# Optimization experiments

Measured on AMD Instinct MI355X. Metric: run time of the kernel, lower is better.

The kernel has to match this reference:

```python
import jax, jax.numpy as jnp
import numpy as np
from jax import lax

NUM_HEAD = 16; M = 2; N = 2; RP = 16; HNR = 8; WNR = 8; NUM_RATIO = 64
ED = 4096           # origin_embed_dim == resize_embed_dim
HD = 4              # head dim (= ED / (NUM_HEAD * 64))
R = 1024 // RP      # 64
THETA = 10.0


def conv2d(x, w, b, stride, pad):
    y = lax.conv_general_dilated(x, w, (stride, stride), ((pad, pad), (pad, pad)),
                                 dimension_numbers=('NCHW', 'OIHW', 'NCHW'))
    return y + b[None, :, None, None]


def layernorm(x, g, b):
    mu = jnp.mean(x, -1, keepdims=True)
    var = jnp.mean((x - mu) ** 2, -1, keepdims=True)
    return (x - mu) * lax.rsqrt(var + 1e-5) * g + b


def l2norm(x):
    n = jnp.sqrt(jnp.sum(x * x, -1, keepdims=True))
    return x / jnp.maximum(n, 1e-12)


def window_partition(x, m, n):
    B, C, H, W = x.shape
    Hp = ((H + m - 1) // m) * m
    Wp = ((W + n - 1) // n) * n
    x = jnp.pad(x, ((0, 0), (0, 0), (0, Hp - H), (0, Wp - W)))
    wh, ww = Hp // m, Wp // n
    x = x.reshape(B, C, m, wh, n, ww).transpose(0, 2, 4, 1, 3, 5).reshape(B * m * n, C, wh, ww)
    return x, (wh, ww), (Hp, Wp)


def window_reverse(x, m, n, paged_shape):
    Hp, Wp = paged_shape
    Bmn, C, wh, ww = x.shape
    B = Bmn // (m * n)
    return x.reshape(B, m, n, C, wh, ww).transpose(0, 3, 1, 4, 2, 5).reshape(B, C, Hp, Wp)


def rope_rotate(t, h, w, theta):
    # 2D axial RoPE over a (h, w) grid flattened row-major; head dim split
    # half for the h-axis and half for the w-axis, consecutive-pair rotation.
    d = t.shape[-1]; dh = d // 2
    freqs = 1.0 / (theta ** (jnp.arange(0, dh, 2, dtype=jnp.float32) / dh))
    px = jnp.repeat(jnp.arange(h, dtype=jnp.float32), w)
    py = jnp.tile(jnp.arange(w, dtype=jnp.float32), h)
    ang = jnp.concatenate([px[:, None] * freqs, py[:, None] * freqs], -1)  # (h*w, dh)
    cos, sin = jnp.cos(ang), jnp.sin(ang)
    tp = t.reshape(t.shape[:-1] + (dh, 2))
    tr = jnp.stack([tp[..., 0] * cos - tp[..., 1] * sin,
                    tp[..., 0] * sin + tp[..., 1] * cos], -1)
    return tr.reshape(t.shape)


def setup_inputs() -> dict:
    key = jax.random.key(0)
    ks = jax.random.split(key, 12)
    s = 0.05
    inp = {
        'x': jax.random.normal(ks[0], (1, 3, 8, 8), jnp.float32),
        'x_conv_w': jax.random.normal(ks[1], (64, 3, 3, 3), jnp.float32) * s,
        'x_conv_b': jnp.zeros((64,), jnp.float32),
        'r_conv_w': jax.random.normal(ks[2], (64, 3, 3, 3), jnp.float32) * s,
        'r_conv_b': jnp.zeros((64,), jnp.float32),
        'patch_w': jax.random.normal(ks[3], (ED, 64, RP, RP), jnp.float32) * s,
        'patch_b': jnp.zeros((ED,), jnp.float32),
        'b_proj_w': jax.random.normal(ks[4], (HD, HD), jnp.float32) * 0.5,
        'b_proj_b': jnp.zeros((HD,), jnp.float32),
        'q_proj_w': jax.random.normal(ks[5], (HD, HD), jnp.float32) * 0.5,
        'q_proj_b': jnp.zeros((HD,), jnp.float32),
        'norm_b_g': jnp.ones((HD,), jnp.float32),
        'norm_b_b': jnp.zeros((HD,), jnp.float32),
        'norm_q_g': jnp.ones((HD,), jnp.float32),
        'norm_q_b': jnp.zeros((HD,), jnp.float32),
        'q_attn_w': jax.random.normal(ks[6], (1, HD), jnp.float32) * 0.5,
        'q_attn_b': jnp.zeros((1,), jnp.float32),
        'pos': jax.random.normal(ks[7], (1, NUM_HEAD, 65536, HD), jnp.float32),
        'proj_w': jax.random.normal(ks[8], (ED, ED, 1, 1), jnp.float32) * s,
        'proj_b': jnp.zeros((ED,), jnp.float32),
    }
    return inp


def reference(x, x_conv_w, x_conv_b, r_conv_w, r_conv_b, patch_w, patch_b,
              b_proj_w, b_proj_b, q_proj_w, q_proj_b,
              norm_b_g, norm_b_b, norm_q_g, norm_q_b,
              q_attn_w, q_attn_b, pos, proj_w, proj_b):
    B, C, H, W = x.shape
    x_feat = conv2d(x, x_conv_w, x_conv_b, 1, 1)                     # (B,64,H,W)
    x_win, xws, x_shape = window_partition(x_feat, M, N)
    pad_h, pad_w = x_shape[0] - H, x_shape[1] - W
    xp = jnp.pad(x, ((0, 0), (0, 0), (0, pad_h), (0, pad_w)))
    res_x = jax.image.resize(xp, (B, 3, 1024, 1024), method='bilinear')
    res_x = conv2d(res_x, r_conv_w, r_conv_b, 1, 1)                  # (B,64,1024,1024)
    res_x_base = conv2d(res_x, patch_w, patch_b, RP, 0)              # (B,4096,64,64)
    C_idx = ED // NUM_RATIO                                          # 64
    rxr = res_x_base.reshape(B, C_idx, HNR, WNR, R, R)
    rxr = rxr.transpose(0, 1, 4, 2, 5, 3).reshape(B, C_idx, R * HNR, R * WNR)  # (B,64,512,512)
    rx_win, rws, rx_shape = window_partition(rxr, M, N)              # (B*4,64,256,256)
    xw = x_win.reshape(B * M * N, NUM_HEAD, -1, xws[0] * xws[1]).swapaxes(-2, -1)  # (B*4,16,Nb,4)
    rw = rx_win.reshape(B * M * N, NUM_HEAD, -1, rws[0] * rws[1]).swapaxes(-2, -1) # (B*4,16,Nq,4)
    b = layernorm(xw, norm_b_g, norm_b_b) @ b_proj_w.T + b_proj_b
    q = layernorm(rw, norm_q_g, norm_q_b) @ q_proj_w.T + q_proj_b
    b_norm = l2norm(b)
    gate = jax.nn.sigmoid(q @ q_attn_w.T + q_attn_b)                 # (B*4,16,Nq,1)
    q = l2norm(q * gate + pos * (1.0 - gate))
    q_rot = rope_rotate(q, rws[0], rws[1], THETA)
    b_rot = rope_rotate(b_norm, xws[0], xws[1], THETA)
    attn = jnp.einsum('bhqd,bhkd->bhqk', q_rot, b_rot)               # (B*4,16,Nq,Nb)
    out_win = attn @ b                                               # (B*4,16,Nq,4)
    out_win = out_win.swapaxes(-2, -1).reshape(B * M * N, -1, rws[0], rws[1])
    n_x = window_reverse(out_win, M, N, rx_shape)                    # (B,64,512,512)
    n_x = n_x.reshape(B, C_idx, R, HNR, R, WNR).transpose(0, 1, 3, 5, 2, 4).reshape(B, -1, R, R)
    x_final = conv2d(n_x + res_x_base, proj_w, proj_b, 1, 0)         # (B,4096,64,64)
    return (x_final, attn)
```

## Files before the change

kernel.cpp:

```cpp
#include <hip/hip_runtime.h>
#include <hip/hip_bf16.h>
#include <math.h>
#include <cstddef>

#define CB_F     2097152ull
#define BIASC_F  4194304ull
#define BBUF_F   4198400ull
#define BROT_F   4202496ull
#define P_F      4206592ull
#define PB_F     20983808ull
#define PRWB_F   29372416ull
#define ATTN_OFF 16777216ull

typedef __attribute__((ext_vector_type(8))) short bf16x8;
typedef __attribute__((ext_vector_type(4))) float f32x4;

#define GLOAD16(gsrc, ldst) \
  __builtin_amdgcn_global_load_lds((const __attribute__((address_space(1))) void*)(gsrc), \
                                   (__attribute__((address_space(3))) void*)(ldst), 16, 0, 0)

__global__ __launch_bounds__(256) void k_xmap_bchain(
    const float* __restrict__ x, __hip_bfloat16* __restrict__ Xmb,
    const float* __restrict__ xcw, const float* __restrict__ xcb,
    const float* __restrict__ bpw, const float* __restrict__ bpb,
    const float* __restrict__ nbg, const float* __restrict__ nbb,
    float* __restrict__ b_buf, float* __restrict__ b_rot)
{
    __shared__ float xs[3][8][8];
    int t = threadIdx.x;
    if (t < 192) xs[t / 64][(t / 8) % 8][t % 8] = x[t];
    __syncthreads();

    if (blockIdx.x < 4096) {
        int s = blockIdx.x, py = s >> 6, px = s & 63;
        __hip_bfloat16 out4[4];
        #pragma unroll
        for (int u = 0; u < 4; ++u) {
            int k = t * 4 + u;
            float val = 0.0f;
            if (k < 972) {
                int ci = k / 324, r = k % 324, m = r / 18, n = r % 18;
                int row = 16 * py + m - 1, col = 16 * px + n - 1;
                if (row >= 0 && row < 1024 && col >= 0 && col < 1024) {
                    float fu = (row + 0.5f) * 0.0078125f - 0.5f;
                    float fv = (col + 0.5f) * 0.0078125f - 0.5f;
                    float fi = floorf(fu), fj = floorf(fv);
                    float tu = fu - fi, tv = fv - fj;
                    int i0 = (int)fi, j0 = (int)fj;
                    int i0c = min(max(i0, 0), 7), i1c = min(max(i0 + 1, 0), 7);
                    int j0c = min(max(j0, 0), 7), j1c = min(max(j0 + 1, 0), 7);
                    val = (xs[ci][i0c][j0c] * (1.f - tv) + xs[ci][i0c][j1c] * tv) * (1.f - tu)
                        + (xs[ci][i1c][j0c] * (1.f - tv) + xs[ci][i1c][j1c] * tv) * tu;
                }
            }
            out4[u] = __float2bfloat16(val);
        }
        *(ushort4*)(Xmb + (size_t)s * 1024 + t * 4) = *(const ushort4*)out4;
        return;
    }

    __shared__ float xf[64][8][8];
    for (int o = t; o < 4096; o += 256) {
        int c = o >> 6, i = (o >> 3) & 7, j = o & 7;
        float acc = xcb[c];
        for (int ic = 0; ic < 3; ++ic)
            for (int ky = 0; ky < 3; ++ky)
                for (int kx = 0; kx < 3; ++kx) {
                    int ii = i - 1 + ky, jj = j - 1 + kx;
                    if (ii >= 0 && ii < 8 && jj >= 0 && jj < 8)
                        acc = fmaf(xs[ic][ii][jj], xcw[((c * 3 + ic) * 3 + ky) * 3 + kx], acc);
                }
        xf[c][i][j] = acc;
    }
    __syncthreads();
    for (int idx = t; idx < 1024; idx += 256) {
        int wi = idx >> 8, h = (idx >> 4) & 15, pp = idx & 15;
        int pr = pp >> 2, pc = pp & 3;
        int gi = 4 * (wi >> 1) + pr, gj = 4 * (wi & 1) + pc;
        float v[4];
        #pragma unroll
        for (int d = 0; d < 4; ++d) v[d] = xf[h * 4 + d][gi][gj];
        float mu = 0.25f * (v[0] + v[1] + v[2] + v[3]);
        float var = 0.25f * ((v[0]-mu)*(v[0]-mu) + (v[1]-mu)*(v[1]-mu) +
                             (v[2]-mu)*(v[2]-mu) + (v[3]-mu)*(v[3]-mu));
        float inv = rsqrtf(var + 1e-5f);
        float xh[4];
        #pragma unroll
        for (int d = 0; d < 4; ++d) xh[d] = (v[d] - mu) * inv * nbg[d] + nbb[d];
        float bv[4];
        #pragma unroll
        for (int d = 0; d < 4; ++d) {
            float a = bpb[d];
            #pragma unroll
            for (int e = 0; e < 4; ++e) a = fmaf(xh[e], bpw[d * 4 + e], a);
            bv[d] = a;
        }
        #pragma unroll
        for (int d = 0; d < 4; ++d) b_buf[idx * 4 + d] = bv[d];
        float nn = sqrtf(bv[0]*bv[0] + bv[1]*bv[1] + bv[2]*bv[2] + bv[3]*bv[3]);
        float in2 = 1.0f / fmaxf(nn, 1e-12f);
        float bn[4];
        #pragma unroll
        for (int d = 0; d < 4; ++d) bn[d] = bv[d] * in2;
        float s0, c0, s1, c1;
        sincosf((float)pr, &s0, &c0);
        sincosf((float)pc, &s1, &c1);
        b_rot[idx * 4 + 0] = bn[0] * c0 - bn[1] * s0;
        b_rot[idx * 4 + 1] = bn[0] * s0 + bn[1] * c0;
        b_rot[idx * 4 + 2] = bn[2] * c1 - bn[3] * s1;
        b_rot[idx * 4 + 3] = bn[2] * s1 + bn[3] * c1;
    }
}

__global__ __launch_bounds__(256) void k_cmat(
    const float* __restrict__ pw, const float* __restrict__ rcw,
    const float* __restrict__ pb, const float* __restrict__ rcb,
    __hip_bfloat16* __restrict__ Cb, float* __restrict__ biasc)
{
    __shared__ __attribute__((aligned(16))) float Ws[64 * 28];
    __shared__ __attribute__((aligned(16))) float Dz[20 * 20 * 28];
    int t = threadIdx.x;
    int w = t >> 6, lane = t & 63;
    int co = blockIdx.x * 4 + w;
    const float* pwc = pw + (size_t)co * 16384;

    for (int i = t; i < 1728; i += 256) Ws[(i / 27) * 28 + (i % 27)] = rcw[i];
    if (t < 64) Ws[t * 28 + 27] = rcb[t];
    for (int i = t; i < 11200; i += 256) Dz[i] = 0.0f;
    __syncthreads();

    float D[4][27];
    #pragma unroll
    for (int q = 0; q < 4; ++q)
        #pragma unroll
        for (int j = 0; j < 27; ++j) D[q][j] = 0.0f;
    float bsum = 0.0f;
    const float* src = pwc + 4 * lane;
    #pragma unroll 4
    for (int c = 0; c < 64; ++c) {
        f32x4 v = *(const f32x4*)(src + c * 256);
        const f32x4* wp = (const f32x4*)&Ws[c * 28];
        #pragma unroll
        for (int q7 = 0; q7 < 7; ++q7) {
            f32x4 wv = wp[q7];
            #pragma unroll
            for (int e = 0; e < 4; ++e) {
                int j = q7 * 4 + e;
                if (j < 27) {
                    #pragma unroll
                    for (int q = 0; q < 4; ++q)
                        D[q][j] = fmaf(wv[e], v[q], D[q][j]);
                } else {
                    bsum = fmaf(wv[e], v[0] + v[1] + v[2] + v[3], bsum);
                }
            }
        }
    }
    #pragma unroll
    for (int s = 32; s; s >>= 1) bsum += __shfl_down(bsum, s, 64);
    if (lane == 0) biasc[co] = pb[co] + bsum;

    for (int p = 0; p < 4; ++p) {
        __syncthreads();
        if (w == p) {
            #pragma unroll
            for (int q = 0; q < 4; ++q) {
                int rs = 4 * lane + q, r = rs >> 4, s2 = rs & 15;
                float* dst = &Dz[((r + 2) * 20 + (s2 + 2)) * 28];
                #pragma unroll
                for (int j = 0; j < 27; ++j) dst[j] = D[q][j];
            }
        }
        __syncthreads();
        int cop = blockIdx.x * 4 + p;
        if (t < 162) {
            int m = t / 9, n0 = (t % 9) * 2;
            float a0[3] = {}, a1[3] = {};
            #pragma unroll
            for (int ci = 0; ci < 3; ++ci)
                #pragma unroll
                for (int ky = 0; ky < 3; ++ky)
                    #pragma unroll
                    for (int kx = 0; kx < 3; ++kx) {
                        int j = ci * 9 + ky * 3 + kx;
                        const float* pz = &Dz[((m - ky + 2) * 20 + (n0 - kx + 2)) * 28 + j];
                        a0[ci] += pz[0];
                        a1[ci] += pz[28];
                    }
            size_t cb = (size_t)cop * 1024;
            #pragma unroll
            for (int ci = 0; ci < 3; ++ci) {
                Cb[cb + ci * 324 + m * 18 + n0]     = __float2bfloat16(a0[ci]);
                Cb[cb + ci * 324 + m * 18 + n0 + 1] = __float2bfloat16(a1[ci]);
            }
        }
        if (t >= 162 && t < 214)
            Cb[(size_t)cop * 1024 + 972 + (t - 162)] = __float2bfloat16(0.0f);
    }
}

__global__ __launch_bounds__(256) void k_cast_bf16(
    const float* __restrict__ in, __hip_bfloat16* __restrict__ out, long n)
{
    long i = ((long)blockIdx.x * 256 + threadIdx.x) * 8;
    if (i >= n) return;
    float4 v0 = *(const float4*)(in + i);
    float4 v1 = *(const float4*)(in + i + 4);
    __hip_bfloat16 h[8] = {__float2bfloat16(v0.x), __float2bfloat16(v0.y),
                           __float2bfloat16(v0.z), __float2bfloat16(v0.w),
                           __float2bfloat16(v1.x), __float2bfloat16(v1.y),
                           __float2bfloat16(v1.z), __float2bfloat16(v1.w)};
    *(ushort4*)(out + i)     = *(const ushort4*)h;
    *(ushort4*)(out + i + 4) = *(const ushort4*)(h + 4);
}

template <int BIASROW>
__global__ __launch_bounds__(512) void gemm_8p(
    const __hip_bfloat16* __restrict__ A, const __hip_bfloat16* __restrict__ B,
    const float* __restrict__ bias, float* __restrict__ C,
    int M, int N, int K)
{
    __shared__ short lds[65536];
    const short* Ag = (const short*)A;
    const short* Bg = (const short*)B;
    int t = threadIdx.x;
    int lane = t & 63;
    int wid = t >> 6;
    int wm = wid >> 2, wn = wid & 3;

    int nwg = gridDim.x * gridDim.y;
    int flat = blockIdx.y * gridDim.x + blockIdx.x;
    int swz = (flat & 7) * (nwg >> 3) + (flat >> 3);
    int bx = swz % gridDim.x, by = swz / gridDim.x;
    int m0 = by * 256, n0 = bx * 256;
    int T = K >> 6;

    int srow = t >> 3;
    int sc = ((t & 7) ^ (srow & 7)) * 8;
    const short* Asrc[4]; const short* Bsrc[4];
    #pragma unroll
    for (int p = 0; p < 4; ++p) {
        Asrc[p] = Ag + (size_t)(m0 + p * 64 + srow) * K + sc;
        Bsrc[p] = Bg + (size_t)(n0 + p * 64 + srow) * K + sc;
    }

    f32x4 acc[8][4] = {};

    #pragma unroll
    for (int u = 0; u < 2; ++u) {
        short* bA = lds + u * 32768;
        short* bB = bA + 16384;
        size_t ko = (size_t)u * 64;
        #pragma unroll
        for (int p = 0; p < 4; ++p) GLOAD16(Asrc[p] + ko, bA + p * 4096 + t * 8);
        #pragma unroll
        for (int p = 0; p < 4; ++p) GLOAD16(Bsrc[p] + ko, bB + p * 4096 + t * 8);
    }

    for (int tt = 0; tt < T; ++tt) {
        if (tt + 1 < T) { asm volatile("s_waitcnt vmcnt(8)" ::: "memory"); }
        else            { asm volatile("s_waitcnt vmcnt(0)" ::: "memory"); }
        __builtin_amdgcn_s_barrier();
        __builtin_amdgcn_sched_barrier(0);

        const char* Asb = (const char*)(lds + (tt & 1) * 32768);
        const char* Bsb = Asb + 32768;
        short* pA = lds + (tt & 1) * 32768;
        short* pB = pA + 16384;
        bool pf = (tt + 2) < T;
        size_t ko = (size_t)(tt + 2) * 64;

        bf16x8 af[4][2], bfr[4][2];
        #pragma unroll
        for (int f = 0; f < 4; ++f) {
            int r = wm * 128 + f * 16 + (lane & 15);
            #pragma unroll
            for (int ks = 0; ks < 2; ++ks) {
                int cb = ks * 64 + (lane >> 4) * 16;
                af[f][ks] = *(const bf16x8*)(Asb + r * 128 + (cb ^ ((r & 7) << 4)));
            }
        }
        #pragma unroll
        for (int g = 0; g < 2; ++g) {
            int r = wn * 64 + g * 16 + (lane & 15);
            #pragma unroll
            for (int ks = 0; ks < 2; ++ks) {
                int cb = ks * 64 + (lane >> 4) * 16;
                bfr[g][ks] = *(const bf16x8*)(Bsb + r * 128 + (cb ^ ((r & 7) << 4)));
            }
        }
        __builtin_amdgcn_s_barrier();
        __builtin_amdgcn_s_setprio(1);
        #pragma unroll
        for (int f = 0; f < 4; ++f)
            #pragma unroll
            for (int g = 0; g < 2; ++g)
                #pragma unroll
                for (int ks = 0; ks < 2; ++ks)
                    acc[f][g] = __builtin_amdgcn_mfma_f32_16x16x32_bf16(
                        af[f][ks], bfr[g][ks], acc[f][g], 0, 0, 0);
        __builtin_amdgcn_s_setprio(0);
        __builtin_amdgcn_s_barrier();
        #pragma unroll
        for (int g = 2; g < 4; ++g) {
            int r = wn * 64 + g * 16 + (lane & 15);
            #pragma unroll
            for (int ks = 0; ks < 2; ++ks) {
                int cb = ks * 64 + (lane >> 4) * 16;
                bfr[g][ks] = *(const bf16x8*)(Bsb + r * 128 + (cb ^ ((r & 7) << 4)));
            }
        }
        __builtin_amdgcn_s_barrier();
        __builtin_amdgcn_s_setprio(1);
        #pragma unroll
        for (int f = 0; f < 4; ++f)
            #pragma unroll
            for (int g = 2; g < 4; ++g)
                #pragma unroll
                for (int ks = 0; ks < 2; ++ks)
                    acc[f][g] = __builtin_amdgcn_mfma_f32_16x16x32_bf16(
                        af[f][ks], bfr[g][ks], acc[f][g], 0, 0, 0);
        __builtin_amdgcn_s_setprio(0);
        __builtin_amdgcn_s_barrier();
        #pragma unroll
        for (int f = 0; f < 4; ++f) {
            int r = wm * 128 + 64 + f * 16 + (lane & 15);
            #pragma unroll
            for (int ks = 0; ks < 2; ++ks) {
                int cb = ks * 64 + (lane >> 4) * 16;
                af[f][ks] = *(const bf16x8*)(Asb + r * 128 + (cb ^ ((r & 7) << 4)));
            }
        }
        if (pf) {
            #pragma unroll
            for (int p = 0; p < 4; ++p) GLOAD16(Bsrc[p] + ko, pB + p * 4096 + t * 8);
        }
        __builtin_amdgcn_s_barrier();
        __builtin_amdgcn_s_setprio(1);
        #pragma unroll
        for (int f = 0; f < 4; ++f)
            #pragma unroll
            for (int g = 0; g < 2; ++g)
                #pragma unroll
                for (int ks = 0; ks < 2; ++ks)
                    acc[4 + f][g] = __builtin_amdgcn_mfma_f32_16x16x32_bf16(
                        af[f][ks], bfr[g][ks], acc[4 + f][g], 0, 0, 0);
        __builtin_amdgcn_s_setprio(0);
        __builtin_amdgcn_s_barrier();
        if (pf) {
            #pragma unroll
            for (int p = 0; p < 4; ++p) GLOAD16(Asrc[p] + ko, pA + p * 4096 + t * 8);
        }
        __builtin_amdgcn_s_setprio(1);
        #pragma unroll
        for (int f = 0; f < 4; ++f)
            #pragma unroll
            for (int g = 2; g < 4; ++g)
                #pragma unroll
                for (int ks = 0; ks < 2; ++ks)
                    acc[4 + f][g] = __builtin_amdgcn_mfma_f32_16x16x32_bf16(
                        af[f][ks], bfr[g][ks], acc[4 + f][g], 0, 0, 0);
        __builtin_amdgcn_s_setprio(0);
    }

    #pragma unroll
    for (int f = 0; f < 8; ++f) {
        #pragma unroll
        for (int g = 0; g < 4; ++g) {
            int col = n0 + wn * 64 + g * 16 + (lane & 15);
            #pragma unroll
            for (int rg = 0; rg < 4; ++rg) {
                int row = m0 + wm * 128 + f * 16 + (lane >> 4) * 4 + rg;
                float bb = BIASROW ? bias[row] : bias[col];
                C[(size_t)row * N + col] = acc[f][g][rg] + bb;
            }
        }
    }
}

__global__ __launch_bounds__(256) void k_attn(
    const float* __restrict__ P, const float* __restrict__ b_buf, const float* __restrict__ b_rot,
    const float* __restrict__ qpw, const float* __restrict__ qpb,
    const float* __restrict__ nqg, const float* __restrict__ nqb,
    const float* __restrict__ qaw, const float* __restrict__ qab,
    const float* __restrict__ pos, __hip_bfloat16* __restrict__ Pb,
    float* __restrict__ attn_out)
{
    __shared__ float bs[16][4], brs[16][4];
    int t = threadIdx.x;
    int wh = blockIdx.y;
    int wi = wh >> 4, h = wh & 15;
    if (t < 64) {
        ((float*)bs)[t]  = b_buf[wh * 64 + t];
        ((float*)brs)[t] = b_rot[wh * 64 + t];
    }
    __syncthreads();
    int p = blockIdx.x * 256 + t;
    int wr = p >> 8, wc = p & 255;
    int gr = ((wi >> 1) << 8) + wr, gc = ((wi & 1) << 8) + wc;
    int y = gr >> 3, hnr = gr & 7, xq = gc >> 3, wnr = gc & 7;
    size_t base = (size_t)(y * 64 + xq) * 4096 + h * 256 + hnr * 8 + wnr;
    float r[4];
    #pragma unroll
    for (int d = 0; d < 4; ++d) r[d] = P[base + (size_t)d * 64];
    float mu = 0.25f * (r[0] + r[1] + r[2] + r[3]);
    float var = 0.25f * ((r[0]-mu)*(r[0]-mu) + (r[1]-mu)*(r[1]-mu) +
                         (r[2]-mu)*(r[2]-mu) + (r[3]-mu)*(r[3]-mu));
    float inv = rsqrtf(var + 1e-5f);
    float xh[4];
    #pragma unroll
    for (int d = 0; d < 4; ++d) xh[d] = (r[d] - mu) * inv * nqg[d] + nqb[d];
    float q4[4];
    #pragma unroll
    for (int d = 0; d < 4; ++d) {
        float a = qpb[d];
        #pragma unroll
        for (int e = 0; e < 4; ++e) a = fmaf(xh[e], qpw[d * 4 + e], a);
        q4[d] = a;
    }
    float z = qab[0];
    #pragma unroll
    for (int d = 0; d < 4; ++d) z = fmaf(q4[d], qaw[d], z);
    float gate = 1.0f / (1.0f + expf(-z));
    float4 pv = *(const float4*)(pos + ((size_t)h * 65536 + p) * 4);
    float v[4];
    v[0] = q4[0] * gate + pv.x * (1.0f - gate);
    v[1] = q4[1] * gate + pv.y * (1.0f - gate);
    v[2] = q4[2] * gate + pv.z * (1.0f - gate);
    v[3] = q4[3] * gate + pv.w * (1.0f - gate);
    float nn = sqrtf(v[0]*v[0] + v[1]*v[1] + v[2]*v[2] + v[3]*v[3]);
    float in2 = 1.0f / fmaxf(nn, 1e-12f);
    #pragma unroll
    for (int d = 0; d < 4; ++d) v[d] *= in2;
    float s0, c0, s1, c1;
    sincosf((float)wr, &s0, &c0);
    sincosf((float)wc, &s1, &c1);
    float qr[4];
    qr[0] = v[0] * c0 - v[1] * s0;
    qr[1] = v[0] * s0 + v[1] * c0;
    qr[2] = v[2] * c1 - v[3] * s1;
    qr[3] = v[2] * s1 + v[3] * c1;
    float arow[16];
    #pragma unroll
    for (int k = 0; k < 16; ++k)
        arow[k] = qr[0] * brs[k][0] + qr[1] * brs[k][1] + qr[2] * brs[k][2] + qr[3] * brs[k][3];
    size_t abase = ((size_t)wh * 65536 + p) * 16;
    #pragma unroll
    for (int kq = 0; kq < 4; ++kq) {
        float4 av;
        av.x = arow[kq * 4 + 0]; av.y = arow[kq * 4 + 1];
        av.z = arow[kq * 4 + 2]; av.w = arow[kq * 4 + 3];
        *(float4*)(attn_out + abase + kq * 4) = av;
    }
    float o[4] = {0.f, 0.f, 0.f, 0.f};
    #pragma unroll
    for (int k = 0; k < 16; ++k) {
        #pragma unroll
        for (int d = 0; d < 4; ++d) o[d] = fmaf(arow[k], bs[k][d], o[d]);
    }
    #pragma unroll
    for (int d = 0; d < 4; ++d)
        Pb[base + (size_t)d * 64] = __float2bfloat16(r[d] + o[d]);
}

extern "C" void kernel_launch(void* const* d_in, const int* in_sizes, int n_in,
                              void* d_out, int out_size, void* d_ws, size_t ws_size,
                              hipStream_t stream)
{
    (void)in_sizes; (void)n_in; (void)out_size; (void)ws_size;
    const float* x    = (const float*)d_in[0];
    const float* xcw  = (const float*)d_in[1];
    const float* xcb  = (const float*)d_in[2];
    const float* rcw  = (const float*)d_in[3];
    const float* rcb  = (const float*)d_in[4];
    const float* pw   = (const float*)d_in[5];
    const float* pb   = (const float*)d_in[6];
    const float* bpw  = (const float*)d_in[7];
    const float* bpb  = (const float*)d_in[8];
    const float* qpw  = (const float*)d_in[9];
    const float* qpb  = (const float*)d_in[10];
    const float* nbg  = (const float*)d_in[11];
    const float* nbb  = (const float*)d_in[12];
    const float* nqg  = (const float*)d_in[13];
    const float* nqb  = (const float*)d_in[14];
    const float* qaw  = (const float*)d_in[15];
    const float* qab  = (const float*)d_in[16];
    const float* pos  = (const float*)d_in[17];
    const float* prw  = (const float*)d_in[18];
    const float* prb  = (const float*)d_in[19];

    float* ws = (float*)d_ws;
    __hip_bfloat16* Xmb   = (__hip_bfloat16*)d_ws;
    __hip_bfloat16* Cb    = (__hip_bfloat16*)(ws + CB_F);
    float*          biasc = ws + BIASC_F;
    float*          b_buf = ws + BBUF_F;
    float*          b_rot = ws + BROT_F;
    float*          P     = ws + P_F;
    __hip_bfloat16* Pb    = (__hip_bfloat16*)(ws + PB_F);
    __hip_bfloat16* prwb  = (__hip_bfloat16*)(ws + PRWB_F);
    float* out = (float*)d_out;

    k_xmap_bchain<<<4097, 256, 0, stream>>>(x, Xmb, xcw, xcb, bpw, bpb, nbg, nbb,
                                            b_buf, b_rot);
    k_cmat<<<1024, 256, 0, stream>>>(pw, rcw, pb, rcb, Cb, biasc);
    gemm_8p<0><<<dim3(16, 16), 512, 0, stream>>>(Xmb, Cb, biasc, P, 4096, 4096, 1024);
    k_attn<<<dim3(256, 64), 256, 0, stream>>>(P, b_buf, b_rot, qpw, qpb, nqg, nqb,
                                              qaw, qab, pos, Pb, out + ATTN_OFF);
    k_cast_bf16<<<8192, 256, 0, stream>>>(prw, prwb, 16777216L);
    gemm_8p<1><<<dim3(16, 16), 512, 0, stream>>>(prwb, Pb, prb, out, 4096, 4096, 4096);
}
```

Baseline: 492.7 us.

## Split k_cmat work across two waves per output channel and shrink LDS staging

Each block of k_cmat now handles 2 output channels instead of 4, with two waves splitting each channel's 256 spatial positions, which halves the per-thread D accumulator from 4x27 to 2x27 floats. The LDS staging buffer shrinks from 28 to 12 floats per position by scattering one input channel at a time across 6 passes, and the bias partial sums are combined through a small shared array. The grid doubles to 2048 blocks. The aim is lower register and LDS pressure so more waves fit per CU, at the cost of more barrier-separated passes and redundant Ws and Dz initialisation per block.

```diff
diff --git a/kernel.cpp b/kernel.cpp
--- a/kernel.cpp
+++ b/kernel.cpp
@@ -14,6 +14,7 @@
 
 typedef __attribute__((ext_vector_type(8))) short bf16x8;
 typedef __attribute__((ext_vector_type(4))) float f32x4;
+typedef __attribute__((ext_vector_type(2))) float f32x2;
 
 #define GLOAD16(gsrc, ldst) \
   __builtin_amdgcn_global_load_lds((const __attribute__((address_space(1))) void*)(gsrc), \
@@ -118,27 +119,29 @@
     __hip_bfloat16* __restrict__ Cb, float* __restrict__ biasc)
 {
     __shared__ __attribute__((aligned(16))) float Ws[64 * 28];
-    __shared__ __attribute__((aligned(16))) float Dz[20 * 20 * 28];
+    __shared__ __attribute__((aligned(16))) float Dz[20 * 20 * 12];
+    __shared__ float red[4];
     int t = threadIdx.x;
     int w = t >> 6, lane = t & 63;
-    int co = blockIdx.x * 4 + w;
+    int co_idx = w >> 1, half = w & 1;
+    int co = blockIdx.x * 2 + co_idx;
     const float* pwc = pw + (size_t)co * 16384;
 
     for (int i = t; i < 1728; i += 256) Ws[(i / 27) * 28 + (i % 27)] = rcw[i];
     if (t < 64) Ws[t * 28 + 27] = rcb[t];
-    for (int i = t; i < 11200; i += 256) Dz[i] = 0.0f;
+    for (int i = t; i < 4800; i += 256) Dz[i] = 0.0f;
     __syncthreads();
 
-    float D[4][27];
-    #pragma unroll
-    for (int q = 0; q < 4; ++q)
+    float D[2][27];
+    #pragma unroll
+    for (int q = 0; q < 2; ++q)
         #pragma unroll
         for (int j = 0; j < 27; ++j) D[q][j] = 0.0f;
     float bsum = 0.0f;
-    const float* src = pwc + 4 * lane;
+    const float* src = pwc + half * 128 + 2 * lane;
     #pragma unroll 4
     for (int c = 0; c < 64; ++c) {
-        f32x4 v = *(const f32x4*)(src + c * 256);
+        f32x2 v = *(const f32x2*)(src + c * 256);
         const f32x4* wp = (const f32x4*)&Ws[c * 28];
         #pragma unroll
         for (int q7 = 0; q7 < 7; ++q7) {
@@ -147,54 +150,53 @@
             for (int e = 0; e < 4; ++e) {
                 int j = q7 * 4 + e;
                 if (j < 27) {
-                    #pragma unroll
-                    for (int q = 0; q < 4; ++q)
-                        D[q][j] = fmaf(wv[e], v[q], D[q][j]);
+                    D[0][j] = fmaf(wv[e], v.x, D[0][j]);
+                    D[1][j] = fmaf(wv[e], v.y, D[1][j]);
                 } else {
-                    bsum = fmaf(wv[e], v[0] + v[1] + v[2] + v[3], bsum);
+                    bsum = fmaf(wv[e], v.x + v.y, bsum);
                 }
             }
         }
     }
     #pragma unroll
     for (int s = 32; s; s >>= 1) bsum += __shfl_down(bsum, s, 64);
-    if (lane == 0) biasc[co] = pb[co] + bsum;
-
-    for (int p = 0; p < 4; ++p) {
+    if (lane == 0) red[w] = bsum;
+    __syncthreads();
+    if (t < 2) biasc[blockIdx.x * 2 + t] = pb[blockIdx.x * 2 + t] + red[t * 2] + red[t * 2 + 1];
+
+    for (int p = 0; p < 6; ++p) {
+        int pc = p >> 1 == 0 ? 0 : 0;  (void)pc;
+        int pco = p / 3, ci = p % 3;
         __syncthreads();
-        if (w == p) {
-            #pragma unroll
-            for (int q = 0; q < 4; ++q) {
-                int rs = 4 * lane + q, r = rs >> 4, s2 = rs & 15;
-                float* dst = &Dz[((r + 2) * 20 + (s2 + 2)) * 28];
+        if (co_idx == pco) {
+            #pragma unroll
+            for (int q = 0; q < 2; ++q) {
+                int rs = half * 128 + 2 * lane + q;
+                int r = rs >> 4, s2 = rs & 15;
+                float* dst = &Dz[((r + 2) * 20 + (s2 + 2)) * 12];
                 #pragma unroll
-                for (int j = 0; j < 27; ++j) dst[j] = D[q][j];
+                for (int u = 0; u < 9; ++u) dst[u] = D[q][ci * 9 + u];
             }
         }
         __syncthreads();
-        int cop = blockIdx.x * 4 + p;
+        int cop = blockIdx.x * 2 + pco;
         if (t < 162) {
             int m = t / 9, n0 = (t % 9) * 2;
-            float a0[3] = {}, a1[3] = {};
-            #pragma unroll
-            for (int ci = 0; ci < 3; ++ci)
+            float a0 = 0.0f, a1 = 0.0f;
+            #pragma unroll
+            for (int ky = 0; ky < 3; ++ky)
                 #pragma unroll
-                for (int ky = 0; ky < 3; ++ky)
-                    #pragma unroll
-                    for (int kx = 0; kx < 3; ++kx) {
-                        int j = ci * 9 + ky * 3 + kx;
-                        const float* pz = &Dz[((m - ky + 2) * 20 + (n0 - kx + 2)) * 28 + j];
-                        a0[ci] += pz[0];
-                        a1[ci] += pz[28];
-                    }
+                for (int kx = 0; kx < 3; ++kx) {
+                    int u = ky * 3 + kx;
+                    const float* pz = &Dz[((m - ky + 2) * 20 + (n0 - kx + 2)) * 12 + u];
+                    a0 += pz[0];
+                    a1 += pz[12];
+                }
             size_t cb = (size_t)cop * 1024;
-            #pragma unroll
-            for (int ci = 0; ci < 3; ++ci) {
-                Cb[cb + ci * 324 + m * 18 + n0]     = __float2bfloat16(a0[ci]);
-                Cb[cb + ci * 324 + m * 18 + n0 + 1] = __float2bfloat16(a1[ci]);
-            }
-        }
-        if (t >= 162 && t < 214)
+            Cb[cb + ci * 324 + m * 18 + n0]     = __float2bfloat16(a0);
+            Cb[cb + ci * 324 + m * 18 + n0 + 1] = __float2bfloat16(a1);
+        }
+        if (ci == 0 && t >= 162 && t < 214)
             Cb[(size_t)cop * 1024 + 972 + (t - 162)] = __float2bfloat16(0.0f);
     }
 }
@@ -502,7 +504,7 @@
 
     k_xmap_bchain<<<4097, 256, 0, stream>>>(x, Xmb, xcw, xcb, bpw, bpb, nbg, nbb,
                                             b_buf, b_rot);
-    k_cmat<<<1024, 256, 0, stream>>>(pw, rcw, pb, rcb, Cb, biasc);
+    k_cmat<<<2048, 256, 0, stream>>>(pw, rcw, pb, rcb, Cb, biasc);
     gemm_8p<0><<<dim3(16, 16), 512, 0, stream>>>(Xmb, Cb, biasc, P, 4096, 4096, 1024);
     k_attn<<<dim3(256, 64), 256, 0, stream>>>(P, b_buf, b_rot, qpw, qpb, nqg, nqb,
                                               qaw, qab, pos, Pb, out + ATTN_OFF);
```

Result: faster. 444.1 us (-9.8%).
